# Kernel optimization log

Measured on AMD Instinct MI355X. Metric: run time of the kernel, lower is better.

Reference implementation:

```python
import jax, jax.numpy as jnp
import numpy as np

EMBED_DIM = 1024
NUM_HEADS = 16
HEAD_DIM = EMBED_DIM // NUM_HEADS
SCALE = float(np.sqrt(HEAD_DIM))


def setup_inputs() -> dict:
    key = jax.random.key(0)
    ks = jax.random.split(key, 7)
    B, S, E = 2, 2048, EMBED_DIM
    query = jax.random.normal(ks[0], (B, S, E), dtype=jnp.float32)
    key_t = jax.random.normal(ks[1], (B, S, E), dtype=jnp.float32)
    value = jax.random.normal(ks[2], (B, S, E), dtype=jnp.float32)
    # nn.Linear(E, E, bias=False): weight shape (out, in); y = x @ W.T
    std = 1.0 / np.sqrt(E)
    Wq = jax.random.uniform(ks[3], (E, E), jnp.float32, -std, std)
    Wk = jax.random.uniform(ks[4], (E, E), jnp.float32, -std, std)
    Wv = jax.random.uniform(ks[5], (E, E), jnp.float32, -std, std)
    Wo = jax.random.uniform(ks[6], (E, E), jnp.float32, -std, std)
    return {"query": query, "key": key_t, "value": value,
            "Wq": Wq, "Wk": Wk, "Wv": Wv, "Wo": Wo}


def reference(query, key, value, Wq, Wk, Wv, Wo):
    B, S, E = query.shape
    H, D = NUM_HEADS, HEAD_DIM
    q = (query @ Wq.T).reshape(B, S, H, D).transpose(0, 2, 1, 3)  # [B,H,S,D]
    k = (key @ Wk.T).reshape(B, S, H, D).transpose(0, 2, 1, 3)
    v = (value @ Wv.T).reshape(B, S, H, D).transpose(0, 2, 1, 3)
    scores = jnp.einsum('bhqd,bhkd->bhqk', q, k) / SCALE  # [B,H,S,S]
    attn = jax.nn.softmax(scores, axis=-1)
    out = jnp.einsum('bhqk,bhkd->bhqd', attn, v)  # [B,H,S,D]
    out = out.transpose(0, 2, 1, 3).reshape(B, S, E)
    return out @ Wo.T
```

## Files before the change

kernel.cpp:

```cpp
#include <hip/hip_runtime.h>
#include <hip/hip_bf16.h>
#include <math.h>

typedef float f32x4 __attribute__((ext_vector_type(4)));
typedef __bf16 bf16x8 __attribute__((ext_vector_type(8)));
typedef unsigned short u16;
typedef u16 u16x8 __attribute__((ext_vector_type(8)));
typedef u16 u16x4 __attribute__((ext_vector_type(4)));

__device__ __forceinline__ u16 f2bf(float f) {
    unsigned u = __builtin_bit_cast(unsigned, f);
    u = (u + 0x7fffu + ((u >> 16) & 1u)) >> 16;
    return (u16)u;
}
__device__ __forceinline__ u16 f2bf_rhu(float f) {
    return (u16)((__builtin_bit_cast(unsigned, f) + 0x8000u) >> 16);
}

#if __has_builtin(__builtin_amdgcn_exp2f)
#define EXP2(x) __builtin_amdgcn_exp2f(x)
#else
#define EXP2(x) exp2f(x)
#endif

__global__ __launch_bounds__(256) void cast_all(
    const float* __restrict__ q, const float* __restrict__ k, const float* __restrict__ v,
    const float* __restrict__ wq, const float* __restrict__ wk, const float* __restrict__ wv,
    const float* __restrict__ wo, u16* __restrict__ dst) {
    int i = blockIdx.x * 256 + threadIdx.x;
    const float* src;
    int off;
    if (i < 3145728) {
        int seg = i >> 20;
        src = (seg == 0) ? q : (seg == 1) ? k : v;
        off = i - (seg << 20);
    } else {
        int j = (i - 3145728) >> 18;
        src = (j == 0) ? wq : (j == 1) ? wk : (j == 2) ? wv : wo;
        off = (i - 3145728) - (j << 18);
    }
    float4 val = ((const float4*)src)[off];
    u16x4 o4;
    o4.x = f2bf(val.x); o4.y = f2bf(val.y); o4.z = f2bf(val.z); o4.w = f2bf(val.w);
    ((u16x4*)dst)[i] = o4;
}

__global__ __launch_bounds__(256) void qkv_gemm(
    const u16* __restrict__ Xq, const u16* __restrict__ Xk, const u16* __restrict__ Xv,
    const u16* __restrict__ Wq, const u16* __restrict__ Wk, const u16* __restrict__ Wv,
    u16* __restrict__ Qo, u16* __restrict__ Ko, u16* __restrict__ Vto) {
    constexpr int K = 1024;
    const int z = blockIdx.z;
    const u16* __restrict__ A = (z == 0) ? Xq : (z == 1) ? Xk : Xv;
    const u16* __restrict__ W = (z == 0) ? Wq : (z == 1) ? Wk : Wv;
    u16* __restrict__ Out = (z == 0) ? Qo : (z == 1) ? Ko : Vto;

    __shared__ __align__(16) u16 As[128 * 32];
    __shared__ __align__(16) u16 Bs[128 * 32];

    const int t = threadIdx.x;
    const int lane = t & 63, wave = t >> 6;
    const int quad = lane >> 4, c = lane & 15;
    const int wr = (wave >> 1) * 64, wc = (wave & 1) * 64;
    const int rowA0 = blockIdx.y * 128;
    const int colB0 = blockIdx.x * 128;
    const int srow = t >> 2;
    const int scol = (t & 3) * 8;
    const u16* pA = A + (rowA0 + srow) * K + scol;
    const u16* pB = W + (colB0 + srow) * K + scol;

    const f32x4 zero4 = {0.f, 0.f, 0.f, 0.f};
    f32x4 acc[4][4];
#pragma unroll
    for (int i = 0; i < 4; ++i)
#pragma unroll
        for (int j = 0; j < 4; ++j) acc[i][j] = zero4;

    for (int kt = 0; kt < K; kt += 32) {
        u16x8 a0 = *(const u16x8*)(pA + kt);
        u16x8 a1 = *(const u16x8*)(pA + 64 * K + kt);
        u16x8 b0 = *(const u16x8*)(pB + kt);
        u16x8 b1 = *(const u16x8*)(pB + 64 * K + kt);
        __syncthreads();
        *(u16x8*)(As + srow * 32 + scol) = a0;
        *(u16x8*)(As + (srow + 64) * 32 + scol) = a1;
        *(u16x8*)(Bs + srow * 32 + scol) = b0;
        *(u16x8*)(Bs + (srow + 64) * 32 + scol) = b1;
        __syncthreads();
        bf16x8 af[4], bfr[4];
#pragma unroll
        for (int i = 0; i < 4; ++i)
            af[i] = *(const bf16x8*)(As + (wr + i * 16 + c) * 32 + quad * 8);
#pragma unroll
        for (int j = 0; j < 4; ++j)
            bfr[j] = *(const bf16x8*)(Bs + (wc + j * 16 + c) * 32 + quad * 8);
        if (z == 2) {
#pragma unroll
            for (int i = 0; i < 4; ++i)
#pragma unroll
                for (int j = 0; j < 4; ++j)
                    acc[i][j] = __builtin_amdgcn_mfma_f32_16x16x32_bf16(bfr[j], af[i], acc[i][j], 0, 0, 0);
        } else {
#pragma unroll
            for (int i = 0; i < 4; ++i)
#pragma unroll
                for (int j = 0; j < 4; ++j)
                    acc[i][j] = __builtin_amdgcn_mfma_f32_16x16x32_bf16(af[i], bfr[j], acc[i][j], 0, 0, 0);
        }
    }

    const float scale = (z == 0) ? 0.18033688011112042f : 1.0f;
#pragma unroll
    for (int i = 0; i < 4; ++i) {
#pragma unroll
        for (int j = 0; j < 4; ++j) {
#pragma unroll
            for (int r = 0; r < 4; ++r) {
                float v = acc[i][j][r];
                if (z == 2) {
                    int n = colB0 + wc + j * 16 + quad * 4 + r;
                    int m = rowA0 + wr + i * 16 + c;
                    int b = m >> 11, s = m & 2047, h = n >> 6, d = n & 63;
                    Out[((((b << 4) | h) << 6) + d) * 2048 + s] = f2bf(v);
                } else {
                    int m = rowA0 + wr + i * 16 + quad * 4 + r;
                    int n = colB0 + wc + j * 16 + c;
                    int b = m >> 11, s = m & 2047, h = n >> 6, d = n & 63;
                    Out[((((b << 4) | h) * 2048 + s) << 6) + d] = f2bf(v * scale);
                }
            }
        }
    }
}

__global__ __launch_bounds__(256) void out_gemm(const u16* __restrict__ A,
                                                const u16* __restrict__ W,
                                                float* __restrict__ Out) {
    constexpr int K = 1024;
    __shared__ __align__(16) u16 As[128 * 32];
    __shared__ __align__(16) u16 Bs[128 * 32];
    const int t = threadIdx.x;
    const int lane = t & 63, wave = t >> 6;
    const int quad = lane >> 4, c = lane & 15;
    const int wr = (wave >> 1) * 64, wc = (wave & 1) * 64;
    const int rowA0 = blockIdx.y * 128;
    const int colB0 = blockIdx.x * 128;
    const int srow = t >> 2;
    const int scol = (t & 3) * 8;
    const u16* pA = A + (rowA0 + srow) * K + scol;
    const u16* pB = W + (colB0 + srow) * K + scol;

    const f32x4 zero4 = {0.f, 0.f, 0.f, 0.f};
    f32x4 acc[4][4];
#pragma unroll
    for (int i = 0; i < 4; ++i)
#pragma unroll
        for (int j = 0; j < 4; ++j) acc[i][j] = zero4;

    for (int kt = 0; kt < K; kt += 32) {
        u16x8 a0 = *(const u16x8*)(pA + kt);
        u16x8 a1 = *(const u16x8*)(pA + 64 * K + kt);
        u16x8 b0 = *(const u16x8*)(pB + kt);
        u16x8 b1 = *(const u16x8*)(pB + 64 * K + kt);
        __syncthreads();
        *(u16x8*)(As + srow * 32 + scol) = a0;
        *(u16x8*)(As + (srow + 64) * 32 + scol) = a1;
        *(u16x8*)(Bs + srow * 32 + scol) = b0;
        *(u16x8*)(Bs + (srow + 64) * 32 + scol) = b1;
        __syncthreads();
        bf16x8 af[4], bfr[4];
#pragma unroll
        for (int i = 0; i < 4; ++i)
            af[i] = *(const bf16x8*)(As + (wr + i * 16 + c) * 32 + quad * 8);
#pragma unroll
        for (int j = 0; j < 4; ++j)
            bfr[j] = *(const bf16x8*)(Bs + (wc + j * 16 + c) * 32 + quad * 8);
#pragma unroll
        for (int i = 0; i < 4; ++i)
#pragma unroll
            for (int j = 0; j < 4; ++j)
                acc[i][j] = __builtin_amdgcn_mfma_f32_16x16x32_bf16(af[i], bfr[j], acc[i][j], 0, 0, 0);
    }
#pragma unroll
    for (int i = 0; i < 4; ++i)
#pragma unroll
        for (int j = 0; j < 4; ++j)
#pragma unroll
            for (int r = 0; r < 4; ++r) {
                int m = rowA0 + wr + i * 16 + quad * 4 + r;
                int n = colB0 + wc + j * 16 + c;
                Out[(m << 10) + n] = acc[i][j][r];
            }
}

__global__ __launch_bounds__(256, 2) void flash_attn(const u16* __restrict__ Qp,
                                                     const u16* __restrict__ Kp,
                                                     const u16* __restrict__ Vt,
                                                     u16* __restrict__ Ob) {
    constexpr int S = 2048;
    constexpr int LD = 72;
    const int bh = blockIdx.y;
    const int b = bh >> 4, h = bh & 15;
    const int t = threadIdx.x, wave = t >> 6, lane = t & 63;
    const int quad = lane >> 4, c = lane & 15;
    const int q0 = blockIdx.x * 128;
    const int qw = q0 + wave * 32;
    const u16* Qb = Qp + (bh * S + qw) * 64;
    const u16* Kb = Kp + (bh * S) * 64;
    const u16* Vb = Vt + bh * 64 * S;

    __shared__ __align__(16) u16 Ks[2][64 * LD];
    __shared__ __align__(16) u16 Vs[2][64 * LD];
    __shared__ __align__(16) u16 Ps[4][32 * LD];
    u16* Pw = &Ps[wave][0];

    bf16x8 qf[2][2];
#pragma unroll
    for (int qt = 0; qt < 2; ++qt)
#pragma unroll
        for (int hf = 0; hf < 2; ++hf)
            qf[qt][hf] = *(const bf16x8*)(Qb + (qt * 16 + c) * 64 + hf * 32 + quad * 8);

    const int r0 = t >> 3, ch = t & 7;
    const u16* kg0 = Kb + r0 * 64 + ch * 8;
    const u16* kg1 = Kb + (r0 + 32) * 64 + ch * 8;
    const u16* vg0 = Vb + r0 * S + ch * 8;
    const u16* vg1 = Vb + (r0 + 32) * S + ch * 8;
    const int d0 = r0 * LD + ch * 8, d1 = (r0 + 32) * LD + ch * 8;

    {
        u16x8 k0 = *(const u16x8*)kg0;
        u16x8 k1 = *(const u16x8*)kg1;
        u16x8 v0 = *(const u16x8*)vg0;
        u16x8 v1 = *(const u16x8*)vg1;
        *(u16x8*)(&Ks[0][d0]) = k0;
        *(u16x8*)(&Ks[0][d1]) = k1;
        *(u16x8*)(&Vs[0][d0]) = v0;
        *(u16x8*)(&Vs[0][d1]) = v1;
    }
    __syncthreads();

    const f32x4 zero4 = {0.f, 0.f, 0.f, 0.f};
    f32x4 o[2][4];
#pragma unroll
    for (int qt = 0; qt < 2; ++qt)
#pragma unroll
        for (int t2 = 0; t2 < 4; ++t2) o[qt][t2] = zero4;
    float lsum[2] = {0.f, 0.f};

    for (int it = 0; it < S / 64; ++it) {
        const int cur = it & 1;
        const u16* Kc = &Ks[cur][0];
        const u16* Vc = &Vs[cur][0];
        u16x8 nk0, nk1, nv0, nv1;
        const bool more = (it + 1 < S / 64);
        if (more) {
            const int kvn = (it + 1) * 64;
            nk0 = *(const u16x8*)(kg0 + kvn * 64);
            nk1 = *(const u16x8*)(kg1 + kvn * 64);
            nv0 = *(const u16x8*)(vg0 + kvn);
            nv1 = *(const u16x8*)(vg1 + kvn);
        }
        f32x4 sc[4][2];
#pragma unroll
        for (int kt = 0; kt < 4; ++kt) {
            bf16x8 kf0 = *(const bf16x8*)(Kc + (kt * 16 + c) * LD + quad * 8);
            bf16x8 kf1 = *(const bf16x8*)(Kc + (kt * 16 + c) * LD + 32 + quad * 8);
#pragma unroll
            for (int qt = 0; qt < 2; ++qt) {
                f32x4 zz = zero4;
                zz = __builtin_amdgcn_mfma_f32_16x16x32_bf16(kf0, qf[qt][0], zz, 0, 0, 0);
                zz = __builtin_amdgcn_mfma_f32_16x16x32_bf16(kf1, qf[qt][1], zz, 0, 0, 0);
                sc[kt][qt] = zz;
            }
        }
#pragma unroll
        for (int kt = 0; kt < 4; ++kt)
#pragma unroll
            for (int qt = 0; qt < 2; ++qt) {
                u16x4 pk;
#pragma unroll
                for (int r = 0; r < 4; ++r) {
                    float p = EXP2(sc[kt][qt][r]);
                    lsum[qt] += p;
                    pk[r] = f2bf_rhu(p);
                }
                *(u16x4*)(Pw + (qt * 16 + c) * LD + kt * 16 + quad * 4) = pk;
            }
        __syncthreads();
        bf16x8 pf[2][2];
#pragma unroll
        for (int qt = 0; qt < 2; ++qt)
#pragma unroll
            for (int kh = 0; kh < 2; ++kh)
                pf[qt][kh] = *(const bf16x8*)(Pw + (qt * 16 + c) * LD + kh * 32 + quad * 8);
#pragma unroll
        for (int t2 = 0; t2 < 4; ++t2) {
            bf16x8 vf0 = *(const bf16x8*)(Vc + (t2 * 16 + c) * LD + quad * 8);
            bf16x8 vf1 = *(const bf16x8*)(Vc + (t2 * 16 + c) * LD + 32 + quad * 8);
#pragma unroll
            for (int qt = 0; qt < 2; ++qt) {
                o[qt][t2] = __builtin_amdgcn_mfma_f32_16x16x32_bf16(pf[qt][0], vf0, o[qt][t2], 0, 0, 0);
                o[qt][t2] = __builtin_amdgcn_mfma_f32_16x16x32_bf16(pf[qt][1], vf1, o[qt][t2], 0, 0, 0);
            }
        }
        if (more) {
            u16* Kn = &Ks[cur ^ 1][0];
            u16* Vn = &Vs[cur ^ 1][0];
            *(u16x8*)(Kn + d0) = nk0;
            *(u16x8*)(Kn + d1) = nk1;
            *(u16x8*)(Vn + d0) = nv0;
            *(u16x8*)(Vn + d1) = nv1;
        }
        __syncthreads();
    }
#pragma unroll
    for (int qt = 0; qt < 2; ++qt) {
        lsum[qt] += __shfl_xor(lsum[qt], 16);
        lsum[qt] += __shfl_xor(lsum[qt], 32);
    }
#pragma unroll
    for (int qt = 0; qt < 2; ++qt)
#pragma unroll
        for (int r = 0; r < 4; ++r) {
            float inv = 1.f / __shfl(lsum[qt], quad * 4 + r);
            int row = qw + qt * 16 + quad * 4 + r;
            int base = ((b * S + row) * 16 + h) * 64;
#pragma unroll
            for (int t2 = 0; t2 < 4; ++t2)
                Ob[base + t2 * 16 + c] = f2bf(o[qt][t2][r] * inv);
        }
}

extern "C" void kernel_launch(void* const* d_in, const int* in_sizes, int n_in,
                              void* d_out, int out_size, void* d_ws, size_t ws_size,
                              hipStream_t stream) {
    const float* q  = (const float*)d_in[0];
    const float* k  = (const float*)d_in[1];
    const float* v  = (const float*)d_in[2];
    const float* wq = (const float*)d_in[3];
    const float* wk = (const float*)d_in[4];
    const float* wv = (const float*)d_in[5];
    const float* wo = (const float*)d_in[6];

    u16* ws = (u16*)d_ws;
    u16* qb  = ws;
    u16* kb  = ws + 4194304;
    u16* vb  = ws + 8388608;
    u16* wqb = ws + 12582912;
    u16* wkb = ws + 13631488;
    u16* wvb = ws + 14680064;
    u16* wob = ws + 15728640;
    u16* Qp  = ws + 16777216;
    u16* Kp  = ws + 20971520;
    u16* Vtp = ws + 25165824;
    u16* Obf = ws + 29360128;

    cast_all<<<16384, 256, 0, stream>>>(q, k, v, wq, wk, wv, wo, ws);

    qkv_gemm<<<dim3(8, 32, 3), 256, 0, stream>>>(qb, kb, vb, wqb, wkb, wvb, Qp, Kp, Vtp);

    flash_attn<<<dim3(16, 32), 256, 0, stream>>>(Qp, Kp, Vtp, Obf);

    out_gemm<<<dim3(8, 32), 256, 0, stream>>>(Obf, wob, (float*)d_out);
}
```

Measured before the change: 241.2 us.

## Use direct global-to-LDS loads with XOR swizzle across GEMMs and attention

Replaces register-staged global loads with global_load_lds DMA into shared memory in the QKV GEMM, output GEMM and flash attention, and replaces padded LDS rows with an XOR-swizzled layout to avoid bank conflicts. The GEMMs move to a K-tile of 64 and get occupancy hints. The output GEMM uses 64-row tiles so it launches twice as many blocks. In attention, P packing uses a byte-permute instruction and a per-wave lgkmcnt wait replaces a block-wide barrier. This removes register staging and barrier costs but relies on the wave-private P buffer and on the async LDS loads being ordered correctly by the remaining barriers.

```diff
diff --git a/kernel.cpp b/kernel.cpp
--- a/kernel.cpp
+++ b/kernel.cpp
@@ -13,8 +13,10 @@
     u = (u + 0x7fffu + ((u >> 16) & 1u)) >> 16;
     return (u16)u;
 }
-__device__ __forceinline__ u16 f2bf_rhu(float f) {
-    return (u16)((__builtin_bit_cast(unsigned, f) + 0x8000u) >> 16);
+__device__ __forceinline__ unsigned pack2_rhu(float a, float b) {
+    return __builtin_amdgcn_perm(__builtin_bit_cast(unsigned, b) + 0x8000u,
+                                 __builtin_bit_cast(unsigned, a) + 0x8000u,
+                                 0x07060302u);
 }
 
 #if __has_builtin(__builtin_amdgcn_exp2f)
@@ -22,6 +24,12 @@
 #else
 #define EXP2(x) exp2f(x)
 #endif
+
+__device__ __forceinline__ void gload16(const u16* g, u16* l) {
+    __builtin_amdgcn_global_load_lds(
+        (const __attribute__((address_space(1))) unsigned int*)(g),
+        (__attribute__((address_space(3))) unsigned int*)(l), 16, 0, 0);
+}
 
 __global__ __launch_bounds__(256) void cast_all(
     const float* __restrict__ q, const float* __restrict__ k, const float* __restrict__ v,
@@ -45,7 +53,7 @@
     ((u16x4*)dst)[i] = o4;
 }
 
-__global__ __launch_bounds__(256) void qkv_gemm(
+__global__ __launch_bounds__(256, 3) void qkv_gemm(
     const u16* __restrict__ Xq, const u16* __restrict__ Xk, const u16* __restrict__ Xv,
     const u16* __restrict__ Wq, const u16* __restrict__ Wk, const u16* __restrict__ Wv,
     u16* __restrict__ Qo, u16* __restrict__ Ko, u16* __restrict__ Vto) {
@@ -55,19 +63,30 @@
     const u16* __restrict__ W = (z == 0) ? Wq : (z == 1) ? Wk : Wv;
     u16* __restrict__ Out = (z == 0) ? Qo : (z == 1) ? Ko : Vto;
 
-    __shared__ __align__(16) u16 As[128 * 32];
-    __shared__ __align__(16) u16 Bs[128 * 32];
+    __shared__ __align__(16) u16 As[128 * 64];
+    __shared__ __align__(16) u16 Bs[128 * 64];
 
     const int t = threadIdx.x;
     const int lane = t & 63, wave = t >> 6;
-    const int quad = lane >> 4, c = lane & 15;
+    const int quad = lane >> 4, c = lane & 15, cx = c & 7;
     const int wr = (wave >> 1) * 64, wc = (wave & 1) * 64;
     const int rowA0 = blockIdx.y * 128;
     const int colB0 = blockIdx.x * 128;
-    const int srow = t >> 2;
-    const int scol = (t & 3) * 8;
-    const u16* pA = A + (rowA0 + srow) * K + scol;
-    const u16* pB = W + (colB0 + srow) * K + scol;
+
+    const int l3 = lane >> 3, l7 = lane & 7;
+    const int chs = (l7 ^ l3) << 3;
+    const u16* gA[4];
+    const u16* gB[4];
+    u16* lA[4];
+    u16* lB[4];
+#pragma unroll
+    for (int i = 0; i < 4; ++i) {
+        int row = wave * 32 + i * 8 + l3;
+        gA[i] = A + (size_t)(rowA0 + row) * K + chs;
+        gB[i] = W + (size_t)(colB0 + row) * K + chs;
+        lA[i] = As + (wave * 256 + i * 64) * 8;
+        lB[i] = Bs + (wave * 256 + i * 64) * 8;
+    }
 
     const f32x4 zero4 = {0.f, 0.f, 0.f, 0.f};
     f32x4 acc[4][4];
@@ -76,36 +95,37 @@
 #pragma unroll
         for (int j = 0; j < 4; ++j) acc[i][j] = zero4;
 
-    for (int kt = 0; kt < K; kt += 32) {
-        u16x8 a0 = *(const u16x8*)(pA + kt);
-        u16x8 a1 = *(const u16x8*)(pA + 64 * K + kt);
-        u16x8 b0 = *(const u16x8*)(pB + kt);
-        u16x8 b1 = *(const u16x8*)(pB + 64 * K + kt);
-        __syncthreads();
-        *(u16x8*)(As + srow * 32 + scol) = a0;
-        *(u16x8*)(As + (srow + 64) * 32 + scol) = a1;
-        *(u16x8*)(Bs + srow * 32 + scol) = b0;
-        *(u16x8*)(Bs + (srow + 64) * 32 + scol) = b1;
-        __syncthreads();
-        bf16x8 af[4], bfr[4];
-#pragma unroll
-        for (int i = 0; i < 4; ++i)
-            af[i] = *(const bf16x8*)(As + (wr + i * 16 + c) * 32 + quad * 8);
-#pragma unroll
-        for (int j = 0; j < 4; ++j)
-            bfr[j] = *(const bf16x8*)(Bs + (wc + j * 16 + c) * 32 + quad * 8);
-        if (z == 2) {
+    for (int kt = 0; kt < K; kt += 64) {
+        __syncthreads();
+#pragma unroll
+        for (int i = 0; i < 4; ++i) {
+            gload16(gA[i] + kt, lA[i]);
+            gload16(gB[i] + kt, lB[i]);
+        }
+        __syncthreads();
+#pragma unroll
+        for (int ks = 0; ks < 2; ++ks) {
+            const int co = ((ks * 4 + quad) ^ cx) << 3;
+            bf16x8 af[4], bfr[4];
 #pragma unroll
             for (int i = 0; i < 4; ++i)
-#pragma unroll
-                for (int j = 0; j < 4; ++j)
-                    acc[i][j] = __builtin_amdgcn_mfma_f32_16x16x32_bf16(bfr[j], af[i], acc[i][j], 0, 0, 0);
-        } else {
-#pragma unroll
-            for (int i = 0; i < 4; ++i)
-#pragma unroll
-                for (int j = 0; j < 4; ++j)
-                    acc[i][j] = __builtin_amdgcn_mfma_f32_16x16x32_bf16(af[i], bfr[j], acc[i][j], 0, 0, 0);
+                af[i] = *(const bf16x8*)(As + (wr + i * 16 + c) * 64 + co);
+#pragma unroll
+            for (int j = 0; j < 4; ++j)
+                bfr[j] = *(const bf16x8*)(Bs + (wc + j * 16 + c) * 64 + co);
+            if (z == 2) {
+#pragma unroll
+                for (int i = 0; i < 4; ++i)
+#pragma unroll
+                    for (int j = 0; j < 4; ++j)
+                        acc[i][j] = __builtin_amdgcn_mfma_f32_16x16x32_bf16(bfr[j], af[i], acc[i][j], 0, 0, 0);
+            } else {
+#pragma unroll
+                for (int i = 0; i < 4; ++i)
+#pragma unroll
+                    for (int j = 0; j < 4; ++j)
+                        acc[i][j] = __builtin_amdgcn_mfma_f32_16x16x32_bf16(af[i], bfr[j], acc[i][j], 0, 0, 0);
+            }
         }
     }
 
@@ -133,56 +153,71 @@
     }
 }
 
-__global__ __launch_bounds__(256) void out_gemm(const u16* __restrict__ A,
-                                                const u16* __restrict__ W,
-                                                float* __restrict__ Out) {
+__global__ __launch_bounds__(256, 2) void out_gemm(const u16* __restrict__ A,
+                                                   const u16* __restrict__ W,
+                                                   float* __restrict__ Out) {
     constexpr int K = 1024;
-    __shared__ __align__(16) u16 As[128 * 32];
-    __shared__ __align__(16) u16 Bs[128 * 32];
+    __shared__ __align__(16) u16 As[64 * 64];
+    __shared__ __align__(16) u16 Bs[128 * 64];
     const int t = threadIdx.x;
     const int lane = t & 63, wave = t >> 6;
-    const int quad = lane >> 4, c = lane & 15;
-    const int wr = (wave >> 1) * 64, wc = (wave & 1) * 64;
-    const int rowA0 = blockIdx.y * 128;
+    const int quad = lane >> 4, c = lane & 15, cx = c & 7;
+    const int wr = (wave >> 1) * 32, wc = (wave & 1) * 64;
+    const int rowA0 = blockIdx.y * 64;
     const int colB0 = blockIdx.x * 128;
-    const int srow = t >> 2;
-    const int scol = (t & 3) * 8;
-    const u16* pA = A + (rowA0 + srow) * K + scol;
-    const u16* pB = W + (colB0 + srow) * K + scol;
+
+    const int l3 = lane >> 3, l7 = lane & 7;
+    const int chs = (l7 ^ l3) << 3;
+    const u16* gA[2];
+    const u16* gB[4];
+    u16* lA[2];
+    u16* lB[4];
+#pragma unroll
+    for (int i = 0; i < 2; ++i) {
+        int row = wave * 16 + i * 8 + l3;
+        gA[i] = A + (size_t)(rowA0 + row) * K + chs;
+        lA[i] = As + (wave * 128 + i * 64) * 8;
+    }
+#pragma unroll
+    for (int i = 0; i < 4; ++i) {
+        int row = wave * 32 + i * 8 + l3;
+        gB[i] = W + (size_t)(colB0 + row) * K + chs;
+        lB[i] = Bs + (wave * 256 + i * 64) * 8;
+    }
 
     const f32x4 zero4 = {0.f, 0.f, 0.f, 0.f};
-    f32x4 acc[4][4];
-#pragma unroll
-    for (int i = 0; i < 4; ++i)
+    f32x4 acc[2][4];
+#pragma unroll
+    for (int i = 0; i < 2; ++i)
 #pragma unroll
         for (int j = 0; j < 4; ++j) acc[i][j] = zero4;
 
-    for (int kt = 0; kt < K; kt += 32) {
-        u16x8 a0 = *(const u16x8*)(pA + kt);
-        u16x8 a1 = *(const u16x8*)(pA + 64 * K + kt);
-        u16x8 b0 = *(const u16x8*)(pB + kt);
-        u16x8 b1 = *(const u16x8*)(pB + 64 * K + kt);
-        __syncthreads();
-        *(u16x8*)(As + srow * 32 + scol) = a0;
-        *(u16x8*)(As + (srow + 64) * 32 + scol) = a1;
-        *(u16x8*)(Bs + srow * 32 + scol) = b0;
-        *(u16x8*)(Bs + (srow + 64) * 32 + scol) = b1;
-        __syncthreads();
-        bf16x8 af[4], bfr[4];
-#pragma unroll
-        for (int i = 0; i < 4; ++i)
-            af[i] = *(const bf16x8*)(As + (wr + i * 16 + c) * 32 + quad * 8);
-#pragma unroll
-        for (int j = 0; j < 4; ++j)
-            bfr[j] = *(const bf16x8*)(Bs + (wc + j * 16 + c) * 32 + quad * 8);
-#pragma unroll
-        for (int i = 0; i < 4; ++i)
+    for (int kt = 0; kt < K; kt += 64) {
+        __syncthreads();
+#pragma unroll
+        for (int i = 0; i < 2; ++i) gload16(gA[i] + kt, lA[i]);
+#pragma unroll
+        for (int i = 0; i < 4; ++i) gload16(gB[i] + kt, lB[i]);
+        __syncthreads();
+#pragma unroll
+        for (int ks = 0; ks < 2; ++ks) {
+            const int co = ((ks * 4 + quad) ^ cx) << 3;
+            bf16x8 af[2], bfr[4];
+#pragma unroll
+            for (int i = 0; i < 2; ++i)
+                af[i] = *(const bf16x8*)(As + (wr + i * 16 + c) * 64 + co);
 #pragma unroll
             for (int j = 0; j < 4; ++j)
-                acc[i][j] = __builtin_amdgcn_mfma_f32_16x16x32_bf16(af[i], bfr[j], acc[i][j], 0, 0, 0);
-    }
-#pragma unroll
-    for (int i = 0; i < 4; ++i)
+                bfr[j] = *(const bf16x8*)(Bs + (wc + j * 16 + c) * 64 + co);
+#pragma unroll
+            for (int i = 0; i < 2; ++i)
+#pragma unroll
+                for (int j = 0; j < 4; ++j)
+                    acc[i][j] = __builtin_amdgcn_mfma_f32_16x16x32_bf16(af[i], bfr[j], acc[i][j], 0, 0, 0);
+        }
+    }
+#pragma unroll
+    for (int i = 0; i < 2; ++i)
 #pragma unroll
         for (int j = 0; j < 4; ++j)
 #pragma unroll
@@ -198,20 +233,18 @@
                                                      const u16* __restrict__ Vt,
                                                      u16* __restrict__ Ob) {
     constexpr int S = 2048;
-    constexpr int LD = 72;
     const int bh = blockIdx.y;
     const int b = bh >> 4, h = bh & 15;
     const int t = threadIdx.x, wave = t >> 6, lane = t & 63;
-    const int quad = lane >> 4, c = lane & 15;
-    const int q0 = blockIdx.x * 128;
-    const int qw = q0 + wave * 32;
+    const int quad = lane >> 4, c = lane & 15, cx = c & 7;
+    const int qw = blockIdx.x * 128 + wave * 32;
     const u16* Qb = Qp + (bh * S + qw) * 64;
     const u16* Kb = Kp + (bh * S) * 64;
     const u16* Vb = Vt + bh * 64 * S;
 
-    __shared__ __align__(16) u16 Ks[2][64 * LD];
-    __shared__ __align__(16) u16 Vs[2][64 * LD];
-    __shared__ __align__(16) u16 Ps[4][32 * LD];
+    __shared__ __align__(16) u16 Ks[2][64 * 64];
+    __shared__ __align__(16) u16 Vs[2][64 * 64];
+    __shared__ __align__(16) u16 Ps[4][32 * 64];
     u16* Pw = &Ps[wave][0];
 
     bf16x8 qf[2][2];
@@ -221,22 +254,22 @@
         for (int hf = 0; hf < 2; ++hf)
             qf[qt][hf] = *(const bf16x8*)(Qb + (qt * 16 + c) * 64 + hf * 32 + quad * 8);
 
-    const int r0 = t >> 3, ch = t & 7;
-    const u16* kg0 = Kb + r0 * 64 + ch * 8;
-    const u16* kg1 = Kb + (r0 + 32) * 64 + ch * 8;
-    const u16* vg0 = Vb + r0 * S + ch * 8;
-    const u16* vg1 = Vb + (r0 + 32) * S + ch * 8;
-    const int d0 = r0 * LD + ch * 8, d1 = (r0 + 32) * LD + ch * 8;
-
-    {
-        u16x8 k0 = *(const u16x8*)kg0;
-        u16x8 k1 = *(const u16x8*)kg1;
-        u16x8 v0 = *(const u16x8*)vg0;
-        u16x8 v1 = *(const u16x8*)vg1;
-        *(u16x8*)(&Ks[0][d0]) = k0;
-        *(u16x8*)(&Ks[0][d1]) = k1;
-        *(u16x8*)(&Vs[0][d0]) = v0;
-        *(u16x8*)(&Vs[0][d1]) = v1;
+    const int l3 = lane >> 3, l7 = lane & 7;
+    const int chs = (l7 ^ l3) << 3;
+    const u16* gK[2];
+    const u16* gV[2];
+    int lbase[2];
+#pragma unroll
+    for (int i = 0; i < 2; ++i) {
+        int row = wave * 16 + i * 8 + l3;
+        gK[i] = Kb + row * 64 + chs;
+        gV[i] = Vb + row * 2048 + chs;
+        lbase[i] = (wave * 128 + i * 64) * 8;
+    }
+#pragma unroll
+    for (int i = 0; i < 2; ++i) {
+        gload16(gK[i], &Ks[0][lbase[i]]);
+        gload16(gV[i], &Vs[0][lbase[i]]);
     }
     __syncthreads();
 
@@ -250,22 +283,22 @@
 
     for (int it = 0; it < S / 64; ++it) {
         const int cur = it & 1;
+        if (it + 1 < S / 64) {
+#pragma unroll
+            for (int i = 0; i < 2; ++i) {
+                gload16(gK[i] + (it + 1) * 4096, &Ks[cur ^ 1][lbase[i]]);
+                gload16(gV[i] + (it + 1) * 64, &Vs[cur ^ 1][lbase[i]]);
+            }
+        }
         const u16* Kc = &Ks[cur][0];
         const u16* Vc = &Vs[cur][0];
-        u16x8 nk0, nk1, nv0, nv1;
-        const bool more = (it + 1 < S / 64);
-        if (more) {
-            const int kvn = (it + 1) * 64;
-            nk0 = *(const u16x8*)(kg0 + kvn * 64);
-            nk1 = *(const u16x8*)(kg1 + kvn * 64);
-            nv0 = *(const u16x8*)(vg0 + kvn);
-            nv1 = *(const u16x8*)(vg1 + kvn);
-        }
+        const int co0 = (quad ^ cx) << 3, co1 = ((4 + quad) ^ cx) << 3;
         f32x4 sc[4][2];
 #pragma unroll
         for (int kt = 0; kt < 4; ++kt) {
-            bf16x8 kf0 = *(const bf16x8*)(Kc + (kt * 16 + c) * LD + quad * 8);
-            bf16x8 kf1 = *(const bf16x8*)(Kc + (kt * 16 + c) * LD + 32 + quad * 8);
+            const int krow = (kt * 16 + c) * 64;
+            bf16x8 kf0 = *(const bf16x8*)(Kc + krow + co0);
+            bf16x8 kf1 = *(const bf16x8*)(Kc + krow + co1);
 #pragma unroll
             for (int qt = 0; qt < 2; ++qt) {
                 f32x4 zz = zero4;
@@ -275,42 +308,38 @@
             }
         }
 #pragma unroll
-        for (int kt = 0; kt < 4; ++kt)
+        for (int kt = 0; kt < 4; ++kt) {
+            const int pchunk = ((kt * 2 + (quad >> 1)) ^ cx) << 3;
 #pragma unroll
             for (int qt = 0; qt < 2; ++qt) {
-                u16x4 pk;
-#pragma unroll
-                for (int r = 0; r < 4; ++r) {
-                    float p = EXP2(sc[kt][qt][r]);
-                    lsum[qt] += p;
-                    pk[r] = f2bf_rhu(p);
-                }
-                *(u16x4*)(Pw + (qt * 16 + c) * LD + kt * 16 + quad * 4) = pk;
-            }
-        __syncthreads();
+                float p0 = EXP2(sc[kt][qt][0]);
+                float p1 = EXP2(sc[kt][qt][1]);
+                float p2 = EXP2(sc[kt][qt][2]);
+                float p3 = EXP2(sc[kt][qt][3]);
+                lsum[qt] += (p0 + p1) + (p2 + p3);
+                uint2 pk;
+                pk.x = pack2_rhu(p0, p1);
+                pk.y = pack2_rhu(p2, p3);
+                *(uint2*)(Pw + (qt * 16 + c) * 64 + pchunk + (quad & 1) * 4) = pk;
+            }
+        }
+        __asm__ __volatile__("s_waitcnt lgkmcnt(0)" ::: "memory");
         bf16x8 pf[2][2];
 #pragma unroll
-        for (int qt = 0; qt < 2; ++qt)
-#pragma unroll
-            for (int kh = 0; kh < 2; ++kh)
-                pf[qt][kh] = *(const bf16x8*)(Pw + (qt * 16 + c) * LD + kh * 32 + quad * 8);
+        for (int qt = 0; qt < 2; ++qt) {
+            pf[qt][0] = *(const bf16x8*)(Pw + (qt * 16 + c) * 64 + co0);
+            pf[qt][1] = *(const bf16x8*)(Pw + (qt * 16 + c) * 64 + co1);
+        }
 #pragma unroll
         for (int t2 = 0; t2 < 4; ++t2) {
-            bf16x8 vf0 = *(const bf16x8*)(Vc + (t2 * 16 + c) * LD + quad * 8);
-            bf16x8 vf1 = *(const bf16x8*)(Vc + (t2 * 16 + c) * LD + 32 + quad * 8);
+            const int vrow = (t2 * 16 + c) * 64;
+            bf16x8 vf0 = *(const bf16x8*)(Vc + vrow + co0);
+            bf16x8 vf1 = *(const bf16x8*)(Vc + vrow + co1);
 #pragma unroll
             for (int qt = 0; qt < 2; ++qt) {
                 o[qt][t2] = __builtin_amdgcn_mfma_f32_16x16x32_bf16(pf[qt][0], vf0, o[qt][t2], 0, 0, 0);
                 o[qt][t2] = __builtin_amdgcn_mfma_f32_16x16x32_bf16(pf[qt][1], vf1, o[qt][t2], 0, 0, 0);
             }
-        }
-        if (more) {
-            u16* Kn = &Ks[cur ^ 1][0];
-            u16* Vn = &Vs[cur ^ 1][0];
-            *(u16x8*)(Kn + d0) = nk0;
-            *(u16x8*)(Kn + d1) = nk1;
-            *(u16x8*)(Vn + d0) = nv0;
-            *(u16x8*)(Vn + d1) = nv1;
         }
         __syncthreads();
     }
@@ -362,5 +391,5 @@
 
     flash_attn<<<dim3(16, 32), 256, 0, stream>>>(Qp, Kp, Vtp, Obf);
 
-    out_gemm<<<dim3(8, 32), 256, 0, stream>>>(Obf, wob, (float*)d_out);
-}
+    out_gemm<<<dim3(8, 64), 256, 0, stream>>>(Obf, wob, (float*)d_out);
+}
```

Result: slower. 287.6 us (+19.2%).
